# Kernel optimization log

Measured on AMD Instinct MI355X. Metric: run time of the kernel, lower is better.

## Reference

```python
import jax, jax.numpy as jnp
import numpy as np

N = 50000   # nodes
E = 1600000 # edges
G = 512     # graphs in batch
IN_DIM, EMBED, H, D = 64, 128, 4, 32
D1, D2, D3 = 128, 64, 16
NEG_SLOPE = 0.2  # DGL GATConv default


def setup_inputs() -> dict:
    key = jax.random.key(0)
    ks = jax.random.split(key, 16)
    def glorot(k, shape):
        fan = shape[0] + shape[-1]
        return jax.random.normal(k, shape, jnp.float32) * jnp.sqrt(2.0 / fan)
    return {
        "feature": jax.random.normal(ks[0], (N, IN_DIM), jnp.float32),
        "src": jax.random.randint(ks[1], (E,), 0, N, jnp.int32),
        "dst": jax.random.randint(ks[2], (E,), 0, N, jnp.int32),
        "graph_ids": jnp.sort(jax.random.randint(ks[3], (N,), 0, G, jnp.int32)),
        "W0": glorot(ks[4], (IN_DIM, EMBED)), "b0": jnp.zeros((EMBED,), jnp.float32),
        "Wfc": glorot(ks[5], (EMBED, H * D)),
        "attn_l": glorot(ks[6], (H, D)), "attn_r": glorot(ks[7], (H, D)),
        "gat_bias": jnp.zeros((H * D,), jnp.float32),
        "W1": glorot(ks[8], (H * D, D1)), "b1": jnp.zeros((D1,), jnp.float32),
        "W2": glorot(ks[9], (D1, D2)), "b2": jnp.zeros((D2,), jnp.float32),
        "W3": glorot(ks[10], (D2, D3)), "b3": jnp.zeros((D3,), jnp.float32),
    }


def reference(feature, src, dst, graph_ids, W0, b0, Wfc, attn_l, attn_r,
              gat_bias, W1, b1, W2, b2, W3, b3):
    # initial dense embed
    h = feature @ W0 + b0                                   # [N, EMBED]
    # GATConv
    feat = (h @ Wfc).reshape(N, H, D)                       # [N,H,D]
    el = jnp.einsum('nhd,hd->nh', feat, attn_l)             # [N,H]
    er = jnp.einsum('nhd,hd->nh', feat, attn_r)
    e = jax.nn.leaky_relu(el[src] + er[dst], NEG_SLOPE)     # [E,H]
    # segment softmax over incoming edges of each dst node
    m = jax.ops.segment_max(e, dst, num_segments=N)         # [N,H]
    ex = jnp.exp(e - m[dst])                                # [E,H]
    denom = jax.ops.segment_sum(ex, dst, num_segments=N)    # [N,H]
    a = ex / denom[dst]                                     # [E,H]
    msg = a[:, :, None] * feat[src]                         # [E,H,D]
    rst = jax.ops.segment_sum(msg, dst, num_segments=N)     # [N,H,D]
    rst = rst + gat_bias.reshape(1, H, D)
    hn = rst.reshape(N, H * D)
    # AvgPooling per graph
    sums = jax.ops.segment_sum(hn, graph_ids, num_segments=G)           # [G,H*D]
    cnts = jax.ops.segment_sum(jnp.ones((N,), hn.dtype), graph_ids, num_segments=G)
    hg = sums / jnp.maximum(cnts, 1.0)[:, None]
    # dense head
    out = jax.nn.elu(hg)
    out = jax.nn.elu(out @ W1 + b1)
    out = jax.nn.elu(out @ W2 + b2)
    out = out @ W3 + b3                                     # [G, D3]
    atten = a[:, :, None]                                   # [E,H,1] like DGL
    return out, atten
```

## Files before the change

kernel.cpp:

```cpp
#include <hip/hip_runtime.h>
#include <hip/hip_fp16.h>
#include <math.h>

#define N_NODES 50000
#define E_EDGES 1600000
#define G_GRAPHS 512
#define IN_DIM 64
#define EMBED 128
#define HD 128
#define NHEAD 4
#define D1 128
#define D2 64
#define D3 16
#define NEG_SLOPE 0.2f
#define NB ((N_NODES + 127) >> 7)
#define PT_TILE 4096
#define PT_BLOCKS ((E_EDGES + PT_TILE - 1) / PT_TILE)
#define FB_CAP 8192

typedef float vfloat4 __attribute__((ext_vector_type(4)));
typedef float vfloat2 __attribute__((ext_vector_type(2)));
typedef unsigned short ushort_t;

static __device__ __forceinline__ float leaky(float x) { return x > 0.f ? x : NEG_SLOPE * x; }

__global__ void __launch_bounds__(256) k0hg(const int* __restrict__ dst, int* __restrict__ ghist,
                                            const float* __restrict__ W0, const float* __restrict__ b0,
                                            const float* __restrict__ Wfc, float* __restrict__ Wc,
                                            float* __restrict__ bc) {
    __shared__ int lh[NB];
    const int t = threadIdx.x;
    if (blockIdx.x < PT_BLOCKS) {
        for (int i = t; i < NB; i += 256) lh[i] = 0;
        __syncthreads();
        const long e0 = (long)blockIdx.x * PT_TILE;
#pragma unroll
        for (int k = 0; k < PT_TILE / 256; ++k) {
            long e = e0 + t + k * 256;
            if (e < E_EDGES) atomicAdd(&lh[dst[e] >> 7], 1);
        }
        __syncthreads();
        for (int i = t; i < NB; i += 256) {
            int v = lh[i];
            if (v) atomicAdd(&ghist[i], v);
        }
    } else {
        int tid = (int)(blockIdx.x - PT_BLOCKS) * 256 + t;
        if (tid < IN_DIM * HD) {
            int i = tid >> 7, j = tid & 127;
            float acc = 0.f;
            for (int k = 0; k < EMBED; ++k) acc += W0[i * EMBED + k] * Wfc[k * HD + j];
            Wc[tid] = acc;
        } else if (tid < IN_DIM * HD + HD) {
            int j = tid - IN_DIM * HD;
            float acc = 0.f;
            for (int k = 0; k < EMBED; ++k) acc += b0[k] * Wfc[k * HD + j];
            bc[j] = acc;
        }
    }
}

__global__ void __launch_bounds__(256) k1_gemm(const float* __restrict__ A,
                                               const float* __restrict__ W,
                                               const float* __restrict__ b,
                                               const float* __restrict__ attn_l,
                                               const float* __restrict__ attn_r,
                                               unsigned char* __restrict__ feat,
                                               float* __restrict__ el,
                                               float* __restrict__ er) {
    __shared__ __align__(16) float Ws[IN_DIM * HD];
    __shared__ __align__(16) float As[64][68];
    const int t = threadIdx.x;
    const int cc = t & 31;
    const int rt = t >> 5;
    const int c0 = cc * 4;
    const int r0 = rt * 8;
    const int row0 = blockIdx.x * 64;

    {
        const float4* Wg = (const float4*)W;
        float4* Wl = (float4*)Ws;
#pragma unroll
        for (int j = 0; j < (IN_DIM * HD / 4) / 256; ++j) Wl[t + j * 256] = Wg[t + j * 256];
    }
#pragma unroll
    for (int j = 0; j < 4; ++j) {
        int i2 = t + j * 256;
        int row = i2 >> 4, kq = i2 & 15;
        int gr = row0 + row;
        float4 v = (gr < N_NODES) ? *(const float4*)(A + (size_t)gr * IN_DIM + kq * 4)
                                  : make_float4(0.f, 0.f, 0.f, 0.f);
        *(float4*)&As[row][kq * 4] = v;
    }
    __syncthreads();

    float acc[8][4];
#pragma unroll
    for (int i = 0; i < 8; ++i)
#pragma unroll
        for (int j = 0; j < 4; ++j) acc[i][j] = 0.f;

    for (int k4 = 0; k4 < IN_DIM / 4; ++k4) {
        vfloat4 w0 = *(const vfloat4*)&Ws[(k4 * 4 + 0) * HD + c0];
        vfloat4 w1 = *(const vfloat4*)&Ws[(k4 * 4 + 1) * HD + c0];
        vfloat4 w2 = *(const vfloat4*)&Ws[(k4 * 4 + 2) * HD + c0];
        vfloat4 w3 = *(const vfloat4*)&Ws[(k4 * 4 + 3) * HD + c0];
#pragma unroll
        for (int i = 0; i < 8; ++i) {
            vfloat4 a = *(const vfloat4*)&As[r0 + i][k4 * 4];
#pragma unroll
            for (int j = 0; j < 4; ++j)
                acc[i][j] += a.x * w0[j] + a.y * w1[j] + a.z * w2[j] + a.w * w3[j];
        }
    }

    {
        vfloat4 bcv = *(const vfloat4*)(b + c0);
#pragma unroll
        for (int i = 0; i < 8; ++i)
#pragma unroll
            for (int j = 0; j < 4; ++j) acc[i][j] += bcv[j];
    }

#pragma unroll
    for (int i = 0; i < 8; ++i) {
        int gr = row0 + r0 + i;
        if (gr < N_NODES) {
            unsigned int ww = __builtin_amdgcn_cvt_pk_fp8_f32(acc[i][0], acc[i][1], 0, false);
            ww = __builtin_amdgcn_cvt_pk_fp8_f32(acc[i][2], acc[i][3], ww, true);
            *(unsigned int*)(feat + (size_t)gr * HD + c0) = ww;
        }
    }

    {
        vfloat4 al = *(const vfloat4*)(attn_l + c0);
        vfloat4 ar = *(const vfloat4*)(attn_r + c0);
        float pl[8], pr[8];
#pragma unroll
        for (int i = 0; i < 8; ++i) {
            pl[i] = acc[i][0] * al[0] + acc[i][1] * al[1] + acc[i][2] * al[2] + acc[i][3] * al[3];
            pr[i] = acc[i][0] * ar[0] + acc[i][1] * ar[1] + acc[i][2] * ar[2] + acc[i][3] * ar[3];
        }
#pragma unroll
        for (int off = 1; off <= 4; off <<= 1) {
#pragma unroll
            for (int i = 0; i < 8; ++i) {
                pl[i] += __shfl_xor(pl[i], off);
                pr[i] += __shfl_xor(pr[i], off);
            }
        }
        if ((cc & 7) == 0) {
            const int h = cc >> 3;
#pragma unroll
            for (int i = 0; i < 8; ++i) {
                int gr = row0 + r0 + i;
                if (gr < N_NODES) {
                    el[gr * 4 + h] = pl[i];
                    er[gr * 4 + h] = pr[i];
                }
            }
        }
    }
}

__global__ void __launch_bounds__(64) sc_scan(const int* __restrict__ ghist,
                                              int* __restrict__ coarse_start,
                                              int* __restrict__ cursorp) {
    const int lane = threadIdx.x;
    int run = 0;
    for (int c = 0; c < (NB + 63) / 64; ++c) {
        int i = c * 64 + lane;
        int v = (i < NB) ? ghist[i] : 0;
        int incl = v;
#pragma unroll
        for (int off = 1; off < 64; off <<= 1) {
            int o = __shfl_up(incl, off, 64);
            if (lane >= off) incl += o;
        }
        if (i < NB) {
            coarse_start[i] = run + incl - v;
            cursorp[i] = run + incl - v;
        }
        run += __shfl(incl, 63, 64);
    }
    if (lane == 0) coarse_start[NB] = E_EDGES;
}

__global__ void __launch_bounds__(256) pt_partition(const int* __restrict__ src,
                                                    const int* __restrict__ dst,
                                                    int* __restrict__ cursorp,
                                                    unsigned int* __restrict__ part) {
    __shared__ int hist[4][NB];
    __shared__ int tot[NB], offs[NB], base_s[NB];
    __shared__ int lcur[4][NB];
    __shared__ unsigned int stage[PT_TILE];
    const int t = threadIdx.x, lane = t & 63, wid = t >> 6;
    const long e0 = (long)blockIdx.x * PT_TILE;
    const int cnt = (int)min((long)PT_TILE, (long)E_EDGES - e0);
    for (int i = t; i < NB; i += 256) {
        hist[0][i] = 0; hist[1][i] = 0; hist[2][i] = 0; hist[3][i] = 0;
    }
    __syncthreads();
    unsigned int v[PT_TILE / 256];
#pragma unroll
    for (int k = 0; k < PT_TILE / 256; ++k) {
        int i = t + k * 256;
        if (i < cnt) {
            int d = dst[e0 + i];
            v[k] = ((unsigned int)d << 16) | (unsigned int)src[e0 + i];
            atomicAdd(&hist[wid][d >> 7], 1);
        } else v[k] = 0xFFFFFFFFu;
    }
    __syncthreads();
    for (int i = t; i < NB; i += 256) {
        int h0 = hist[0][i], h1 = hist[1][i], h2 = hist[2][i], h3 = hist[3][i];
        hist[0][i] = 0; hist[1][i] = h0; hist[2][i] = h0 + h1; hist[3][i] = h0 + h1 + h2;
        tot[i] = h0 + h1 + h2 + h3;
    }
    __syncthreads();
    if (wid == 0) {
        int run = 0;
        for (int c = 0; c < (NB + 63) / 64; ++c) {
            int i = c * 64 + lane;
            int vv = (i < NB) ? tot[i] : 0;
            int incl = vv;
#pragma unroll
            for (int off = 1; off < 64; off <<= 1) {
                int o = __shfl_up(incl, off, 64);
                if (lane >= off) incl += o;
            }
            if (i < NB) offs[i] = run + incl - vv;
            run += __shfl(incl, 63, 64);
        }
    }
    __syncthreads();
    for (int i = t; i < NB; i += 256) {
        int tt = tot[i];
        base_s[i] = tt ? atomicAdd(&cursorp[i], tt) : 0;
        int ob = offs[i];
        lcur[0][i] = ob + hist[0][i];
        lcur[1][i] = ob + hist[1][i];
        lcur[2][i] = ob + hist[2][i];
        lcur[3][i] = ob + hist[3][i];
    }
    __syncthreads();
#pragma unroll
    for (int k = 0; k < PT_TILE / 256; ++k) {
        if (v[k] != 0xFFFFFFFFu) {
            int b = v[k] >> 23;
            int pos = atomicAdd(&lcur[wid][b], 1);
            stage[pos] = v[k];
        }
    }
    __syncthreads();
    for (int i = t; i < cnt; i += 256) {
        unsigned int p = stage[i];
        int b = p >> 23;
        part[base_s[b] + (i - offs[b])] = p & 0x7FFFFFu;
    }
}

__global__ void __launch_bounds__(256) fb_fill(const unsigned int* __restrict__ part,
                                               const int* __restrict__ coarse_start,
                                               int* __restrict__ rowstart,
                                               ushort_t* __restrict__ csr_src) {
    const int b = blockIdx.x, t = threadIdx.x, lane = t & 63, wid = t >> 6;
    const int s0 = coarse_start[b], s1 = coarse_start[b + 1];
    const int cnt = s1 - s0;
    __shared__ int degl[4][128], totl[128], offl[128], curl[4][128];
    __shared__ ushort_t lsrc[FB_CAP];
    if (t < 128) { degl[0][t] = 0; degl[1][t] = 0; degl[2][t] = 0; degl[3][t] = 0; }
    __syncthreads();
    for (int i = t; i < cnt; i += 256) {
        unsigned int p = part[s0 + i];
        atomicAdd(&degl[wid][p >> 16], 1);
    }
    __syncthreads();
    if (t < 128) {
        int d0 = degl[0][t], d1 = degl[1][t], d2 = degl[2][t], d3 = degl[3][t];
        degl[0][t] = 0; degl[1][t] = d0; degl[2][t] = d0 + d1; degl[3][t] = d0 + d1 + d2;
        totl[t] = d0 + d1 + d2 + d3;
    }
    __syncthreads();
    if (wid == 0) {
        int run = 0;
        for (int c = 0; c < 2; ++c) {
            int i = c * 64 + lane;
            int vv = totl[i];
            int incl = vv;
#pragma unroll
            for (int off = 1; off < 64; off <<= 1) {
                int o = __shfl_up(incl, off, 64);
                if (lane >= off) incl += o;
            }
            offl[i] = run + incl - vv;
            run += __shfl(incl, 63, 64);
        }
    }
    __syncthreads();
    if (t < 128) {
        int ob = offl[t];
        curl[0][t] = ob + degl[0][t];
        curl[1][t] = ob + degl[1][t];
        curl[2][t] = ob + degl[2][t];
        curl[3][t] = ob + degl[3][t];
        int node = (b << 7) + t;
        if (node < N_NODES) rowstart[node] = s0 + ob;
    }
    if (b == 0 && t == 0) rowstart[N_NODES] = E_EDGES;
    __syncthreads();
    if (cnt <= FB_CAP) {
        for (int i = t; i < cnt; i += 256) {
            unsigned int p = part[s0 + i];
            int pos = atomicAdd(&curl[wid][p >> 16], 1);
            lsrc[pos] = (ushort_t)(p & 0xFFFFu);
        }
        __syncthreads();
        for (int i = t; i < cnt; i += 256) csr_src[s0 + i] = lsrc[i];
    } else {
        for (int i = t; i < cnt; i += 256) {
            unsigned int p = part[s0 + i];
            int pos = atomicAdd(&curl[wid][p >> 16], 1);
            csr_src[s0 + pos] = (ushort_t)(p & 0xFFFFu);
        }
    }
}

__global__ void __launch_bounds__(256) k6_aggregate(
    const ushort_t* __restrict__ csr_src, const int* __restrict__ rowstart,
    const float* __restrict__ el, const float* __restrict__ er,
    const unsigned char* __restrict__ feat, const float* __restrict__ gat_bias,
    float* __restrict__ er_rd, float* __restrict__ hn) {
    __shared__ uint2 s_pk[4][64][4];
    const int wid = threadIdx.x >> 6;
    const int lane = threadIdx.x & 63;
    const int n = blockIdx.x * 4 + wid;
    if (n >= N_NODES) return;
    const int start = rowstart[n];
    const int end = rowstart[n + 1];
    const int deg = end - start;

    const int e0 = lane >> 2;
    const int h = lane & 3;
    const float erh = er[n * 4 + h];
    float sm = 0.f;
    for (int base = 0; base < deg; base += 16) {
        const int e = base + e0;
        const bool v = e < deg;
        if (v) {
            const int s = csr_src[start + e];
            const float ex = __expf(leaky(el[s * 4 + h] + erh));
            sm += ex;
            if (e < 64)
                s_pk[wid][e][h] = make_uint2((unsigned int)s << 7, __float_as_uint(ex));
        }
    }
#pragma unroll
    for (int off = 4; off <= 32; off <<= 1) sm += __shfl_xor(sm, off);
    const float rd = sm > 0.f ? 1.f / sm : 0.f;
    if (lane < 4) {
        er_rd[(size_t)n * 8 + lane] = erh;
        er_rd[(size_t)n * 8 + 4 + lane] = rd;
    }

    const int g4 = lane >> 4, gl = lane & 15;
    const int h2 = gl >> 2;
    const float rdh = __shfl(rd, h2);
    vfloat2 acc0 = {0.f, 0.f}, acc1 = {0.f, 0.f}, acc2 = {0.f, 0.f}, acc3 = {0.f, 0.f};

    if (deg <= 64) {
        const uint2* pk = &s_pk[wid][0][h2];
        const unsigned char* fg = feat + (gl << 3);
        int idx = g4;
        for (; idx + 4 < deg; idx += 8) {
            const uint2 pA = pk[idx * 4];
            const uint2 pB = pk[(idx + 4) * 4];
            const uint2 wA = *(const uint2*)(fg + pA.x);
            const uint2 wB = *(const uint2*)(fg + pB.x);
            const float exA = __uint_as_float(pA.y);
            const float exB = __uint_as_float(pB.y);
            const vfloat2 eA = {exA, exA}, eB = {exB, exB};
            acc0 += eA * __builtin_amdgcn_cvt_pk_f32_fp8(wA.x, false);
            acc1 += eA * __builtin_amdgcn_cvt_pk_f32_fp8(wA.x, true);
            acc2 += eA * __builtin_amdgcn_cvt_pk_f32_fp8(wA.y, false);
            acc3 += eA * __builtin_amdgcn_cvt_pk_f32_fp8(wA.y, true);
            acc0 += eB * __builtin_amdgcn_cvt_pk_f32_fp8(wB.x, false);
            acc1 += eB * __builtin_amdgcn_cvt_pk_f32_fp8(wB.x, true);
            acc2 += eB * __builtin_amdgcn_cvt_pk_f32_fp8(wB.y, false);
            acc3 += eB * __builtin_amdgcn_cvt_pk_f32_fp8(wB.y, true);
        }
        if (idx < deg) {
            const uint2 p = pk[idx * 4];
            const uint2 w = *(const uint2*)(fg + p.x);
            const float ex = __uint_as_float(p.y);
            const vfloat2 ev = {ex, ex};
            acc0 += ev * __builtin_amdgcn_cvt_pk_f32_fp8(w.x, false);
            acc1 += ev * __builtin_amdgcn_cvt_pk_f32_fp8(w.x, true);
            acc2 += ev * __builtin_amdgcn_cvt_pk_f32_fp8(w.y, false);
            acc3 += ev * __builtin_amdgcn_cvt_pk_f32_fp8(w.y, true);
        }
    } else {
        const float erh2 = __shfl(erh, h2);
        const unsigned char* fg = feat + (gl << 3);
        for (int e = start + g4; e < end; e += 4) {
            const unsigned int s = csr_src[e];
            const float ex = __expf(leaky(el[s * 4 + h2] + erh2));
            const vfloat2 ev = {ex, ex};
            const uint2 w = *(const uint2*)(fg + ((size_t)s << 7));
            acc0 += ev * __builtin_amdgcn_cvt_pk_f32_fp8(w.x, false);
            acc1 += ev * __builtin_amdgcn_cvt_pk_f32_fp8(w.x, true);
            acc2 += ev * __builtin_amdgcn_cvt_pk_f32_fp8(w.y, false);
            acc3 += ev * __builtin_amdgcn_cvt_pk_f32_fp8(w.y, true);
        }
    }
    {
        const vfloat2 rv = {rdh, rdh};
        acc0 *= rv; acc1 *= rv; acc2 *= rv; acc3 *= rv;
    }
#pragma unroll
    for (int off = 16; off <= 32; off <<= 1) {
        acc0.x += __shfl_xor(acc0.x, off);
        acc0.y += __shfl_xor(acc0.y, off);
        acc1.x += __shfl_xor(acc1.x, off);
        acc1.y += __shfl_xor(acc1.y, off);
        acc2.x += __shfl_xor(acc2.x, off);
        acc2.y += __shfl_xor(acc2.y, off);
        acc3.x += __shfl_xor(acc3.x, off);
        acc3.y += __shfl_xor(acc3.y, off);
    }
    if (lane < 16) {
        const float4 b0 = ((const float4*)gat_bias)[gl * 2];
        const float4 b1 = ((const float4*)gat_bias)[gl * 2 + 1];
        float4* hp = (float4*)(hn + (size_t)n * HD + gl * 8);
        hp[0] = make_float4(acc0.x + b0.x, acc0.y + b0.y, acc1.x + b0.z, acc1.y + b0.w);
        hp[1] = make_float4(acc2.x + b1.x, acc2.y + b1.y, acc3.x + b1.z, acc3.y + b1.w);
    }
}

__global__ void __launch_bounds__(256) k6b_attn(
    const int* __restrict__ src, const int* __restrict__ dst,
    const float* __restrict__ el, const float* __restrict__ er_rd,
    float* __restrict__ a_out) {
    int e = blockIdx.x * 256 + threadIdx.x;
    if (e >= E_EDGES) return;
    const int s = src[e], d = dst[e];
    const float4 el4 = *(const float4*)(el + s * 4);
    const float4 er4 = *(const float4*)(er_rd + (size_t)d * 8);
    const float4 r4 = *(const float4*)(er_rd + (size_t)d * 8 + 4);
    vfloat4 a;
    a.x = __expf(leaky(el4.x + er4.x)) * r4.x;
    a.y = __expf(leaky(el4.y + er4.y)) * r4.y;
    a.z = __expf(leaky(el4.z + er4.z)) * r4.z;
    a.w = __expf(leaky(el4.w + er4.w)) * r4.w;
    __builtin_nontemporal_store(a, (vfloat4*)a_out + e);
}

__global__ void __launch_bounds__(512) k7_pool_mlp(
    const float* __restrict__ hn, const int* __restrict__ graph_ids,
    const float* __restrict__ W1, const float* __restrict__ b1,
    const float* __restrict__ W2, const float* __restrict__ b2,
    const float* __restrict__ W3, const float* __restrict__ b3,
    float* __restrict__ out) {
    const int g = blockIdx.x, t = threadIdx.x;
    const int tt = t & 127, part = t >> 7;
    __shared__ int bounds[2];
    __shared__ double pool[4][128];
    __shared__ double x[128], y[128];
    if (t < 2) {
        const int target = g + t;
        int lo = 0, hi = N_NODES;
        while (lo < hi) {
            int mid = (lo + hi) >> 1;
            if (graph_ids[mid] < target) lo = mid + 1; else hi = mid;
        }
        bounds[t] = lo;
    }
    __syncthreads();
    const int lo = bounds[0], hi = bounds[1];
    double s = 0.0;
    for (int n = lo + part; n < hi; n += 4) s += (double)hn[(size_t)n * HD + tt];
    pool[part][tt] = s;
    __syncthreads();
    if (t < 128) {
        const double cnt = (double)(hi - lo);
        const double sum = pool[0][t] + pool[1][t] + pool[2][t] + pool[3][t];
        const double v = sum / fmax(cnt, 1.0);
        x[t] = v > 0.0 ? v : expm1(v);
    }
    __syncthreads();
    if (t < 128) {
        double acc = (double)b1[t];
        for (int k = 0; k < HD; ++k) acc += x[k] * (double)W1[k * D1 + t];
        y[t] = acc > 0.0 ? acc : expm1(acc);
    }
    __syncthreads();
    if (t < D2) {
        double a2 = (double)b2[t];
        for (int k = 0; k < D1; ++k) a2 += y[k] * (double)W2[k * D2 + t];
        x[t] = a2 > 0.0 ? a2 : expm1(a2);
    }
    __syncthreads();
    if (t < D3) {
        double a3 = (double)b3[t];
        for (int k = 0; k < D2; ++k) a3 += x[k] * (double)W3[k * D3 + t];
        out[g * D3 + t] = (float)a3;
    }
}

extern "C" void kernel_launch(void* const* d_in, const int* in_sizes, int n_in,
                              void* d_out, int out_size, void* d_ws, size_t ws_size,
                              hipStream_t stream) {
    const float* feature = (const float*)d_in[0];
    const int* src = (const int*)d_in[1];
    const int* dst = (const int*)d_in[2];
    const int* graph_ids = (const int*)d_in[3];
    const float* W0 = (const float*)d_in[4];
    const float* b0 = (const float*)d_in[5];
    const float* Wfc = (const float*)d_in[6];
    const float* attn_l = (const float*)d_in[7];
    const float* attn_r = (const float*)d_in[8];
    const float* gat_bias = (const float*)d_in[9];
    const float* W1 = (const float*)d_in[10];
    const float* b1 = (const float*)d_in[11];
    const float* W2 = (const float*)d_in[12];
    const float* b2 = (const float*)d_in[13];
    const float* W3 = (const float*)d_in[14];
    const float* b3 = (const float*)d_in[15];

    char* ws = (char*)d_ws;
    size_t off = 0;
    auto carve = [&](size_t bytes) -> void* {
        void* p = ws + off;
        off += (bytes + 255) & ~(size_t)255;
        return p;
    };
    int* ghist = (int*)carve((size_t)NB * 4);
    const size_t zero_span = off;
    int* coarse_start = (int*)carve((size_t)(NB + 1) * 4);
    int* cursorp = (int*)carve((size_t)NB * 4);
    float* Wc = (float*)carve((size_t)IN_DIM * HD * 4);
    float* bc = (float*)carve((size_t)HD * 4);
    unsigned char* feat = (unsigned char*)carve((size_t)N_NODES * HD);
    float* el = (float*)carve((size_t)N_NODES * 4 * 4);
    float* er = (float*)carve((size_t)N_NODES * 4 * 4);
    float* er_rd = (float*)carve((size_t)N_NODES * 8 * 4);
    int* rowstart = (int*)carve((size_t)(N_NODES + 1) * 4);
    unsigned int* part = (unsigned int*)carve((size_t)E_EDGES * 4);
    ushort_t* csr_src = (ushort_t*)carve((size_t)E_EDGES * 2);

    float* out = (float*)d_out;
    float* hn = out + G_GRAPHS * D3;
    float* a_out = hn;

    (void)hipMemsetAsync(d_ws, 0, zero_span, stream);
    k0hg<<<PT_BLOCKS + 33, 256, 0, stream>>>(dst, ghist, W0, b0, Wfc, Wc, bc);
    k1_gemm<<<(N_NODES + 63) / 64, 256, 0, stream>>>(feature, Wc, bc, attn_l, attn_r,
                                                     feat, el, er);
    sc_scan<<<1, 64, 0, stream>>>(ghist, coarse_start, cursorp);
    pt_partition<<<PT_BLOCKS, 256, 0, stream>>>(src, dst, cursorp, part);
    fb_fill<<<NB, 256, 0, stream>>>(part, coarse_start, rowstart, csr_src);
    k6_aggregate<<<(N_NODES + 3) / 4, 256, 0, stream>>>(csr_src, rowstart, el, er, feat,
                                                        gat_bias, er_rd, hn);
    k7_pool_mlp<<<G_GRAPHS, 512, 0, stream>>>(hn, graph_ids, W1, b1, W2, b2, W3, b3, out);
    k6b_attn<<<(E_EDGES + 255) / 256, 256, 0, stream>>>(src, dst, el, er_rd, a_out);
}
```

Measured before the change: 250.4 us.

## Fuse attention output into aggregate kernel via original-edge-index permutation

Carries each edge's original index through the partition and CSR build, so the aggregate kernel can scatter normalized attention weights straight into the output. This removes the separate per-edge attention kernel, which re-gathered el and er_rd by src and dst. It also unrolls the score computation for low-degree nodes and reshapes the feature-accumulation loop into four-wide batches. In exchange it adds 4-byte original-index streams written and read in two kernels, scattered 4-byte stores to a_out, and moves hn into the workspace.

```diff
diff --git a/kernel.cpp b/kernel.cpp
--- a/kernel.cpp
+++ b/kernel.cpp
@@ -189,11 +189,13 @@
 __global__ void __launch_bounds__(256) pt_partition(const int* __restrict__ src,
                                                     const int* __restrict__ dst,
                                                     int* __restrict__ cursorp,
-                                                    unsigned int* __restrict__ part) {
+                                                    unsigned int* __restrict__ part,
+                                                    unsigned int* __restrict__ parto) {
     __shared__ int hist[4][NB];
     __shared__ int tot[NB], offs[NB], base_s[NB];
     __shared__ int lcur[4][NB];
     __shared__ unsigned int stage[PT_TILE];
+    __shared__ unsigned int stage2[PT_TILE];
     const int t = threadIdx.x, lane = t & 63, wid = t >> 6;
     const long e0 = (long)blockIdx.x * PT_TILE;
     const int cnt = (int)min((long)PT_TILE, (long)E_EDGES - e0);
@@ -250,20 +252,25 @@
             int b = v[k] >> 23;
             int pos = atomicAdd(&lcur[wid][b], 1);
             stage[pos] = v[k];
+            stage2[pos] = (unsigned int)(e0 + t + k * 256);
         }
     }
     __syncthreads();
     for (int i = t; i < cnt; i += 256) {
         unsigned int p = stage[i];
         int b = p >> 23;
-        part[base_s[b] + (i - offs[b])] = p & 0x7FFFFFu;
+        int o = base_s[b] + (i - offs[b]);
+        part[o] = p & 0x7FFFFFu;
+        parto[o] = stage2[i];
     }
 }
 
 __global__ void __launch_bounds__(256) fb_fill(const unsigned int* __restrict__ part,
+                                               const unsigned int* __restrict__ parto,
                                                const int* __restrict__ coarse_start,
                                                int* __restrict__ rowstart,
-                                               ushort_t* __restrict__ csr_src) {
+                                               ushort_t* __restrict__ csr_src,
+                                               int* __restrict__ csr_orig) {
     const int b = blockIdx.x, t = threadIdx.x, lane = t & 63, wid = t >> 6;
     const int s0 = coarse_start[b], s1 = coarse_start[b + 1];
     const int cnt = s1 - s0;
@@ -312,25 +319,30 @@
     if (cnt <= FB_CAP) {
         for (int i = t; i < cnt; i += 256) {
             unsigned int p = part[s0 + i];
+            int orig = (int)parto[s0 + i];
             int pos = atomicAdd(&curl[wid][p >> 16], 1);
             lsrc[pos] = (ushort_t)(p & 0xFFFFu);
+            csr_orig[s0 + pos] = orig;
         }
         __syncthreads();
         for (int i = t; i < cnt; i += 256) csr_src[s0 + i] = lsrc[i];
     } else {
         for (int i = t; i < cnt; i += 256) {
             unsigned int p = part[s0 + i];
+            int orig = (int)parto[s0 + i];
             int pos = atomicAdd(&curl[wid][p >> 16], 1);
             csr_src[s0 + pos] = (ushort_t)(p & 0xFFFFu);
+            csr_orig[s0 + pos] = orig;
         }
     }
 }
 
 __global__ void __launch_bounds__(256) k6_aggregate(
-    const ushort_t* __restrict__ csr_src, const int* __restrict__ rowstart,
+    const ushort_t* __restrict__ csr_src, const int* __restrict__ csr_orig,
+    const int* __restrict__ rowstart,
     const float* __restrict__ el, const float* __restrict__ er,
     const unsigned char* __restrict__ feat, const float* __restrict__ gat_bias,
-    float* __restrict__ er_rd, float* __restrict__ hn) {
+    float* __restrict__ hn, float* __restrict__ a_out) {
     __shared__ uint2 s_pk[4][64][4];
     const int wid = threadIdx.x >> 6;
     const int lane = threadIdx.x & 63;
@@ -344,23 +356,66 @@
     const int h = lane & 3;
     const float erh = er[n * 4 + h];
     float sm = 0.f;
-    for (int base = 0; base < deg; base += 16) {
-        const int e = base + e0;
-        const bool v = e < deg;
-        if (v) {
-            const int s = csr_src[start + e];
-            const float ex = __expf(leaky(el[s * 4 + h] + erh));
-            sm += ex;
-            if (e < 64)
-                s_pk[wid][e][h] = make_uint2((unsigned int)s << 7, __float_as_uint(ex));
+    bool vA = false, vB = false, vC = false, vD = false;
+    float xA = 0.f, xB = 0.f, xC = 0.f, xD = 0.f;
+    int oA = 0, oB = 0, oC = 0, oD = 0;
+    if (deg <= 64) {
+        vA = e0 < deg; vB = e0 + 16 < deg; vC = e0 + 32 < deg; vD = e0 + 48 < deg;
+        const int iA = start + (vA ? e0 : 0);
+        const int iB = start + (vB ? e0 + 16 : 0);
+        const int iC = start + (vC ? e0 + 32 : 0);
+        const int iD = start + (vD ? e0 + 48 : 0);
+        const int sA = csr_src[iA], sB = csr_src[iB], sC = csr_src[iC], sD = csr_src[iD];
+        oA = csr_orig[iA]; oB = csr_orig[iB]; oC = csr_orig[iC]; oD = csr_orig[iD];
+        const float lA = el[sA * 4 + h];
+        const float lB = el[sB * 4 + h];
+        const float lC = el[sC * 4 + h];
+        const float lD = el[sD * 4 + h];
+        xA = vA ? __expf(leaky(lA + erh)) : 0.f;
+        xB = vB ? __expf(leaky(lB + erh)) : 0.f;
+        xC = vC ? __expf(leaky(lC + erh)) : 0.f;
+        xD = vD ? __expf(leaky(lD + erh)) : 0.f;
+        sm = xA + xB + xC + xD;
+        if (vA) s_pk[wid][e0][h]      = make_uint2((unsigned int)sA << 7, __float_as_uint(xA));
+        if (vB) s_pk[wid][e0 + 16][h] = make_uint2((unsigned int)sB << 7, __float_as_uint(xB));
+        if (vC) s_pk[wid][e0 + 32][h] = make_uint2((unsigned int)sC << 7, __float_as_uint(xC));
+        if (vD) s_pk[wid][e0 + 48][h] = make_uint2((unsigned int)sD << 7, __float_as_uint(xD));
+    } else {
+        for (int base = 0; base < deg; base += 16) {
+            const int e = base + e0;
+            if (e < deg) {
+                const int s = csr_src[start + e];
+                const float ex = __expf(leaky(el[s * 4 + h] + erh));
+                sm += ex;
+                if (e < 64)
+                    s_pk[wid][e][h] = make_uint2((unsigned int)s << 7, __float_as_uint(ex));
+            }
         }
     }
 #pragma unroll
     for (int off = 4; off <= 32; off <<= 1) sm += __shfl_xor(sm, off);
     const float rd = sm > 0.f ? 1.f / sm : 0.f;
-    if (lane < 4) {
-        er_rd[(size_t)n * 8 + lane] = erh;
-        er_rd[(size_t)n * 8 + 4 + lane] = rd;
+
+    if (deg <= 64) {
+        if (vA) a_out[(size_t)oA * 4 + h] = xA * rd;
+        if (vB) a_out[(size_t)oB * 4 + h] = xB * rd;
+        if (vC) a_out[(size_t)oC * 4 + h] = xC * rd;
+        if (vD) a_out[(size_t)oD * 4 + h] = xD * rd;
+    } else {
+        const float er0 = __shfl(erh, 0), er1 = __shfl(erh, 1);
+        const float er2 = __shfl(erh, 2), er3 = __shfl(erh, 3);
+        const float rd0 = __shfl(rd, 0), rd1 = __shfl(rd, 1);
+        const float rd2 = __shfl(rd, 2), rd3 = __shfl(rd, 3);
+        for (int e = start + lane; e < end; e += 64) {
+            const int s = csr_src[e], o = csr_orig[e];
+            const float4 elv = *(const float4*)(el + s * 4);
+            vfloat4 a;
+            a.x = __expf(leaky(elv.x + er0)) * rd0;
+            a.y = __expf(leaky(elv.y + er1)) * rd1;
+            a.z = __expf(leaky(elv.z + er2)) * rd2;
+            a.w = __expf(leaky(elv.w + er3)) * rd3;
+            *(vfloat4*)(a_out + (size_t)o * 4) = a;
+        }
     }
 
     const int g4 = lane >> 4, gl = lane & 15;
@@ -371,33 +426,50 @@
     if (deg <= 64) {
         const uint2* pk = &s_pk[wid][0][h2];
         const unsigned char* fg = feat + (gl << 3);
-        int idx = g4;
-        for (; idx + 4 < deg; idx += 8) {
-            const uint2 pA = pk[idx * 4];
-            const uint2 pB = pk[(idx + 4) * 4];
-            const uint2 wA = *(const uint2*)(fg + pA.x);
-            const uint2 wB = *(const uint2*)(fg + pB.x);
-            const float exA = __uint_as_float(pA.y);
-            const float exB = __uint_as_float(pB.y);
-            const vfloat2 eA = {exA, exA}, eB = {exB, exB};
-            acc0 += eA * __builtin_amdgcn_cvt_pk_f32_fp8(wA.x, false);
-            acc1 += eA * __builtin_amdgcn_cvt_pk_f32_fp8(wA.x, true);
-            acc2 += eA * __builtin_amdgcn_cvt_pk_f32_fp8(wA.y, false);
-            acc3 += eA * __builtin_amdgcn_cvt_pk_f32_fp8(wA.y, true);
-            acc0 += eB * __builtin_amdgcn_cvt_pk_f32_fp8(wB.x, false);
-            acc1 += eB * __builtin_amdgcn_cvt_pk_f32_fp8(wB.x, true);
-            acc2 += eB * __builtin_amdgcn_cvt_pk_f32_fp8(wB.y, false);
-            acc3 += eB * __builtin_amdgcn_cvt_pk_f32_fp8(wB.y, true);
-        }
-        if (idx < deg) {
-            const uint2 p = pk[idx * 4];
-            const uint2 w = *(const uint2*)(fg + p.x);
-            const float ex = __uint_as_float(p.y);
-            const vfloat2 ev = {ex, ex};
-            acc0 += ev * __builtin_amdgcn_cvt_pk_f32_fp8(w.x, false);
-            acc1 += ev * __builtin_amdgcn_cvt_pk_f32_fp8(w.x, true);
-            acc2 += ev * __builtin_amdgcn_cvt_pk_f32_fp8(w.y, false);
-            acc3 += ev * __builtin_amdgcn_cvt_pk_f32_fp8(w.y, true);
+        for (int base = g4; base < deg; base += 16) {
+            const int E1 = base + 4 < deg ? base + 4 : base;
+            const int E2 = base + 8 < deg ? base + 8 : base;
+            const int E3 = base + 12 < deg ? base + 12 : base;
+            const uint2 p0 = pk[base * 4];
+            const uint2 p1 = pk[E1 * 4];
+            const uint2 p2 = pk[E2 * 4];
+            const uint2 p3 = pk[E3 * 4];
+            const uint2 w0 = *(const uint2*)(fg + p0.x);
+            const uint2 w1 = *(const uint2*)(fg + p1.x);
+            const uint2 w2 = *(const uint2*)(fg + p2.x);
+            const uint2 w3 = *(const uint2*)(fg + p3.x);
+            const float y0 = __uint_as_float(p0.y);
+            const float y1 = base + 4 < deg ? __uint_as_float(p1.y) : 0.f;
+            const float y2 = base + 8 < deg ? __uint_as_float(p2.y) : 0.f;
+            const float y3 = base + 12 < deg ? __uint_as_float(p3.y) : 0.f;
+            {
+                const vfloat2 e = {y0, y0};
+                acc0 += e * __builtin_amdgcn_cvt_pk_f32_fp8(w0.x, false);
+                acc1 += e * __builtin_amdgcn_cvt_pk_f32_fp8(w0.x, true);
+                acc2 += e * __builtin_amdgcn_cvt_pk_f32_fp8(w0.y, false);
+                acc3 += e * __builtin_amdgcn_cvt_pk_f32_fp8(w0.y, true);
+            }
+            {
+                const vfloat2 e = {y1, y1};
+                acc0 += e * __builtin_amdgcn_cvt_pk_f32_fp8(w1.x, false);
+                acc1 += e * __builtin_amdgcn_cvt_pk_f32_fp8(w1.x, true);
+                acc2 += e * __builtin_amdgcn_cvt_pk_f32_fp8(w1.y, false);
+                acc3 += e * __builtin_amdgcn_cvt_pk_f32_fp8(w1.y, true);
+            }
+            {
+                const vfloat2 e = {y2, y2};
+                acc0 += e * __builtin_amdgcn_cvt_pk_f32_fp8(w2.x, false);
+                acc1 += e * __builtin_amdgcn_cvt_pk_f32_fp8(w2.x, true);
+                acc2 += e * __builtin_amdgcn_cvt_pk_f32_fp8(w2.y, false);
+                acc3 += e * __builtin_amdgcn_cvt_pk_f32_fp8(w2.y, true);
+            }
+            {
+                const vfloat2 e = {y3, y3};
+                acc0 += e * __builtin_amdgcn_cvt_pk_f32_fp8(w3.x, false);
+                acc1 += e * __builtin_amdgcn_cvt_pk_f32_fp8(w3.x, true);
+                acc2 += e * __builtin_amdgcn_cvt_pk_f32_fp8(w3.y, false);
+                acc3 += e * __builtin_amdgcn_cvt_pk_f32_fp8(w3.y, true);
+            }
         }
     } else {
         const float erh2 = __shfl(erh, h2);
@@ -435,24 +507,6 @@
         hp[0] = make_float4(acc0.x + b0.x, acc0.y + b0.y, acc1.x + b0.z, acc1.y + b0.w);
         hp[1] = make_float4(acc2.x + b1.x, acc2.y + b1.y, acc3.x + b1.z, acc3.y + b1.w);
     }
-}
-
-__global__ void __launch_bounds__(256) k6b_attn(
-    const int* __restrict__ src, const int* __restrict__ dst,
-    const float* __restrict__ el, const float* __restrict__ er_rd,
-    float* __restrict__ a_out) {
-    int e = blockIdx.x * 256 + threadIdx.x;
-    if (e >= E_EDGES) return;
-    const int s = src[e], d = dst[e];
-    const float4 el4 = *(const float4*)(el + s * 4);
-    const float4 er4 = *(const float4*)(er_rd + (size_t)d * 8);
-    const float4 r4 = *(const float4*)(er_rd + (size_t)d * 8 + 4);
-    vfloat4 a;
-    a.x = __expf(leaky(el4.x + er4.x)) * r4.x;
-    a.y = __expf(leaky(el4.y + er4.y)) * r4.y;
-    a.z = __expf(leaky(el4.z + er4.z)) * r4.z;
-    a.w = __expf(leaky(el4.w + er4.w)) * r4.w;
-    __builtin_nontemporal_store(a, (vfloat4*)a_out + e);
 }
 
 __global__ void __launch_bounds__(512) k7_pool_mlp(
@@ -543,24 +597,24 @@
     unsigned char* feat = (unsigned char*)carve((size_t)N_NODES * HD);
     float* el = (float*)carve((size_t)N_NODES * 4 * 4);
     float* er = (float*)carve((size_t)N_NODES * 4 * 4);
-    float* er_rd = (float*)carve((size_t)N_NODES * 8 * 4);
     int* rowstart = (int*)carve((size_t)(N_NODES + 1) * 4);
     unsigned int* part = (unsigned int*)carve((size_t)E_EDGES * 4);
+    unsigned int* parto = (unsigned int*)carve((size_t)E_EDGES * 4);
     ushort_t* csr_src = (ushort_t*)carve((size_t)E_EDGES * 2);
+    int* csr_orig = (int*)carve((size_t)E_EDGES * 4);
+    float* hn = (float*)carve((size_t)N_NODES * HD * 4);
 
     float* out = (float*)d_out;
-    float* hn = out + G_GRAPHS * D3;
-    float* a_out = hn;
+    float* a_out = out + G_GRAPHS * D3;
 
     (void)hipMemsetAsync(d_ws, 0, zero_span, stream);
     k0hg<<<PT_BLOCKS + 33, 256, 0, stream>>>(dst, ghist, W0, b0, Wfc, Wc, bc);
     k1_gemm<<<(N_NODES + 63) / 64, 256, 0, stream>>>(feature, Wc, bc, attn_l, attn_r,
                                                      feat, el, er);
     sc_scan<<<1, 64, 0, stream>>>(ghist, coarse_start, cursorp);
-    pt_partition<<<PT_BLOCKS, 256, 0, stream>>>(src, dst, cursorp, part);
-    fb_fill<<<NB, 256, 0, stream>>>(part, coarse_start, rowstart, csr_src);
-    k6_aggregate<<<(N_NODES + 3) / 4, 256, 0, stream>>>(csr_src, rowstart, el, er, feat,
-                                                        gat_bias, er_rd, hn);
+    pt_partition<<<PT_BLOCKS, 256, 0, stream>>>(src, dst, cursorp, part, parto);
+    fb_fill<<<NB, 256, 0, stream>>>(part, parto, coarse_start, rowstart, csr_src, csr_orig);
+    k6_aggregate<<<(N_NODES + 3) / 4, 256, 0, stream>>>(csr_src, csr_orig, rowstart, el, er,
+                                                        feat, gat_bias, hn, a_out);
     k7_pool_mlp<<<G_GRAPHS, 512, 0, stream>>>(hn, graph_ids, W1, b1, W2, b2, W3, b3, out);
-    k6b_attn<<<(E_EDGES + 255) / 256, 256, 0, stream>>>(src, dst, el, er_rd, a_out);
-}
+}
```

Result: no change. 248.0 us (-1.0%).

## Split GAT aggregation into two head-halves per node, unroll edge loads

Applied to the files above, without the earlier changes.

The aggregation kernel now launches twice as many blocks, and each half handles two of the four heads (64 feature bytes) per destination node. The softmax-denominator pass for low-degree nodes is unrolled into four independent gathers, and the weighted-sum loop issues four loads per iteration to expose more memory parallelism. fb_fill now processes two coarse buckets per block, and the partition tile is doubled. The cost is that each half recomputes the edge exponentials and denominators, and CSR indices are read twice.

```diff
diff --git a/kernel.cpp b/kernel.cpp
--- a/kernel.cpp
+++ b/kernel.cpp
@@ -14,9 +14,10 @@
 #define D3 16
 #define NEG_SLOPE 0.2f
 #define NB ((N_NODES + 127) >> 7)
-#define PT_TILE 4096
+#define PT_TILE 8192
 #define PT_BLOCKS ((E_EDGES + PT_TILE - 1) / PT_TILE)
 #define FB_CAP 8192
+#define K6_NBLK ((N_NODES + 3) / 4)
 
 typedef float vfloat4 __attribute__((ext_vector_type(4)));
 typedef float vfloat2 __attribute__((ext_vector_type(2)));
@@ -264,65 +265,70 @@
                                                const int* __restrict__ coarse_start,
                                                int* __restrict__ rowstart,
                                                ushort_t* __restrict__ csr_src) {
-    const int b = blockIdx.x, t = threadIdx.x, lane = t & 63, wid = t >> 6;
-    const int s0 = coarse_start[b], s1 = coarse_start[b + 1];
-    const int cnt = s1 - s0;
+    const int t = threadIdx.x, lane = t & 63, wid = t >> 6;
     __shared__ int degl[4][128], totl[128], offl[128], curl[4][128];
     __shared__ ushort_t lsrc[FB_CAP];
-    if (t < 128) { degl[0][t] = 0; degl[1][t] = 0; degl[2][t] = 0; degl[3][t] = 0; }
-    __syncthreads();
-    for (int i = t; i < cnt; i += 256) {
-        unsigned int p = part[s0 + i];
-        atomicAdd(&degl[wid][p >> 16], 1);
-    }
-    __syncthreads();
-    if (t < 128) {
-        int d0 = degl[0][t], d1 = degl[1][t], d2 = degl[2][t], d3 = degl[3][t];
-        degl[0][t] = 0; degl[1][t] = d0; degl[2][t] = d0 + d1; degl[3][t] = d0 + d1 + d2;
-        totl[t] = d0 + d1 + d2 + d3;
-    }
-    __syncthreads();
-    if (wid == 0) {
-        int run = 0;
-        for (int c = 0; c < 2; ++c) {
-            int i = c * 64 + lane;
-            int vv = totl[i];
-            int incl = vv;
-#pragma unroll
-            for (int off = 1; off < 64; off <<= 1) {
-                int o = __shfl_up(incl, off, 64);
-                if (lane >= off) incl += o;
-            }
-            offl[i] = run + incl - vv;
-            run += __shfl(incl, 63, 64);
-        }
-    }
-    __syncthreads();
-    if (t < 128) {
-        int ob = offl[t];
-        curl[0][t] = ob + degl[0][t];
-        curl[1][t] = ob + degl[1][t];
-        curl[2][t] = ob + degl[2][t];
-        curl[3][t] = ob + degl[3][t];
-        int node = (b << 7) + t;
-        if (node < N_NODES) rowstart[node] = s0 + ob;
-    }
-    if (b == 0 && t == 0) rowstart[N_NODES] = E_EDGES;
-    __syncthreads();
-    if (cnt <= FB_CAP) {
+    if (blockIdx.x == 0 && t == 0) rowstart[N_NODES] = E_EDGES;
+    for (int sub = 0; sub < 2; ++sub) {
+        const int b = (int)blockIdx.x * 2 + sub;
+        if (b >= NB) break;
+        const int s0 = coarse_start[b], s1 = coarse_start[b + 1];
+        const int cnt = s1 - s0;
+        if (t < 128) { degl[0][t] = 0; degl[1][t] = 0; degl[2][t] = 0; degl[3][t] = 0; }
+        __syncthreads();
         for (int i = t; i < cnt; i += 256) {
             unsigned int p = part[s0 + i];
-            int pos = atomicAdd(&curl[wid][p >> 16], 1);
-            lsrc[pos] = (ushort_t)(p & 0xFFFFu);
-        }
-        __syncthreads();
-        for (int i = t; i < cnt; i += 256) csr_src[s0 + i] = lsrc[i];
-    } else {
-        for (int i = t; i < cnt; i += 256) {
-            unsigned int p = part[s0 + i];
-            int pos = atomicAdd(&curl[wid][p >> 16], 1);
-            csr_src[s0 + pos] = (ushort_t)(p & 0xFFFFu);
-        }
+            atomicAdd(&degl[wid][p >> 16], 1);
+        }
+        __syncthreads();
+        if (t < 128) {
+            int d0 = degl[0][t], d1 = degl[1][t], d2 = degl[2][t], d3 = degl[3][t];
+            degl[0][t] = 0; degl[1][t] = d0; degl[2][t] = d0 + d1; degl[3][t] = d0 + d1 + d2;
+            totl[t] = d0 + d1 + d2 + d3;
+        }
+        __syncthreads();
+        if (wid == 0) {
+            int run = 0;
+            for (int c = 0; c < 2; ++c) {
+                int i = c * 64 + lane;
+                int vv = totl[i];
+                int incl = vv;
+#pragma unroll
+                for (int off = 1; off < 64; off <<= 1) {
+                    int o = __shfl_up(incl, off, 64);
+                    if (lane >= off) incl += o;
+                }
+                offl[i] = run + incl - vv;
+                run += __shfl(incl, 63, 64);
+            }
+        }
+        __syncthreads();
+        if (t < 128) {
+            int ob = offl[t];
+            curl[0][t] = ob + degl[0][t];
+            curl[1][t] = ob + degl[1][t];
+            curl[2][t] = ob + degl[2][t];
+            curl[3][t] = ob + degl[3][t];
+            int node = (b << 7) + t;
+            if (node < N_NODES) rowstart[node] = s0 + ob;
+        }
+        __syncthreads();
+        if (cnt <= FB_CAP) {
+            for (int i = t; i < cnt; i += 256) {
+                unsigned int p = part[s0 + i];
+                int pos = atomicAdd(&curl[wid][p >> 16], 1);
+                lsrc[pos] = (ushort_t)(p & 0xFFFFu);
+            }
+            __syncthreads();
+            for (int i = t; i < cnt; i += 256) csr_src[s0 + i] = lsrc[i];
+        } else {
+            for (int i = t; i < cnt; i += 256) {
+                unsigned int p = part[s0 + i];
+                int pos = atomicAdd(&curl[wid][p >> 16], 1);
+                csr_src[s0 + pos] = (ushort_t)(p & 0xFFFFu);
+            }
+        }
+        __syncthreads();
     }
 }
 
@@ -334,7 +340,8 @@
     __shared__ uint2 s_pk[4][64][4];
     const int wid = threadIdx.x >> 6;
     const int lane = threadIdx.x & 63;
-    const int n = blockIdx.x * 4 + wid;
+    const int half = (int)(blockIdx.x >= K6_NBLK);
+    const int n = ((int)blockIdx.x - half * K6_NBLK) * 4 + wid;
     if (n >= N_NODES) return;
     const int start = rowstart[n];
     const int end = rowstart[n + 1];
@@ -344,78 +351,106 @@
     const int h = lane & 3;
     const float erh = er[n * 4 + h];
     float sm = 0.f;
-    for (int base = 0; base < deg; base += 16) {
-        const int e = base + e0;
-        const bool v = e < deg;
-        if (v) {
-            const int s = csr_src[start + e];
-            const float ex = __expf(leaky(el[s * 4 + h] + erh));
-            sm += ex;
-            if (e < 64)
-                s_pk[wid][e][h] = make_uint2((unsigned int)s << 7, __float_as_uint(ex));
+    if (deg <= 64) {
+        const bool vA = e0 < deg, vB = e0 + 16 < deg, vC = e0 + 32 < deg, vD = e0 + 48 < deg;
+        const int iA = start + (vA ? e0 : 0);
+        const int iB = start + (vB ? e0 + 16 : 0);
+        const int iC = start + (vC ? e0 + 32 : 0);
+        const int iD = start + (vD ? e0 + 48 : 0);
+        const int sA = csr_src[iA], sB = csr_src[iB], sC = csr_src[iC], sD = csr_src[iD];
+        const float lA = el[sA * 4 + h];
+        const float lB = el[sB * 4 + h];
+        const float lC = el[sC * 4 + h];
+        const float lD = el[sD * 4 + h];
+        const float xA = vA ? __expf(leaky(lA + erh)) : 0.f;
+        const float xB = vB ? __expf(leaky(lB + erh)) : 0.f;
+        const float xC = vC ? __expf(leaky(lC + erh)) : 0.f;
+        const float xD = vD ? __expf(leaky(lD + erh)) : 0.f;
+        sm = xA + xB + xC + xD;
+        if (vA) s_pk[wid][e0][h]      = make_uint2((unsigned int)sA << 7, __float_as_uint(xA));
+        if (vB) s_pk[wid][e0 + 16][h] = make_uint2((unsigned int)sB << 7, __float_as_uint(xB));
+        if (vC) s_pk[wid][e0 + 32][h] = make_uint2((unsigned int)sC << 7, __float_as_uint(xC));
+        if (vD) s_pk[wid][e0 + 48][h] = make_uint2((unsigned int)sD << 7, __float_as_uint(xD));
+    } else {
+        for (int base = 0; base < deg; base += 16) {
+            const int e = base + e0;
+            if (e < deg) {
+                const int s = csr_src[start + e];
+                const float ex = __expf(leaky(el[s * 4 + h] + erh));
+                sm += ex;
+                if (e < 64)
+                    s_pk[wid][e][h] = make_uint2((unsigned int)s << 7, __float_as_uint(ex));
+            }
         }
     }
 #pragma unroll
     for (int off = 4; off <= 32; off <<= 1) sm += __shfl_xor(sm, off);
     const float rd = sm > 0.f ? 1.f / sm : 0.f;
-    if (lane < 4) {
+    if (half == 0 && lane < 4) {
         er_rd[(size_t)n * 8 + lane] = erh;
         er_rd[(size_t)n * 8 + 4 + lane] = rd;
     }
 
     const int g4 = lane >> 4, gl = lane & 15;
-    const int h2 = gl >> 2;
+    const int h2 = (half << 1) | (gl >> 3);
     const float rdh = __shfl(rd, h2);
-    vfloat2 acc0 = {0.f, 0.f}, acc1 = {0.f, 0.f}, acc2 = {0.f, 0.f}, acc3 = {0.f, 0.f};
+    vfloat2 acc0 = {0.f, 0.f}, acc1 = {0.f, 0.f};
 
     if (deg <= 64) {
         const uint2* pk = &s_pk[wid][0][h2];
-        const unsigned char* fg = feat + (gl << 3);
-        int idx = g4;
-        for (; idx + 4 < deg; idx += 8) {
-            const uint2 pA = pk[idx * 4];
-            const uint2 pB = pk[(idx + 4) * 4];
-            const uint2 wA = *(const uint2*)(fg + pA.x);
-            const uint2 wB = *(const uint2*)(fg + pB.x);
-            const float exA = __uint_as_float(pA.y);
-            const float exB = __uint_as_float(pB.y);
-            const vfloat2 eA = {exA, exA}, eB = {exB, exB};
-            acc0 += eA * __builtin_amdgcn_cvt_pk_f32_fp8(wA.x, false);
-            acc1 += eA * __builtin_amdgcn_cvt_pk_f32_fp8(wA.x, true);
-            acc2 += eA * __builtin_amdgcn_cvt_pk_f32_fp8(wA.y, false);
-            acc3 += eA * __builtin_amdgcn_cvt_pk_f32_fp8(wA.y, true);
-            acc0 += eB * __builtin_amdgcn_cvt_pk_f32_fp8(wB.x, false);
-            acc1 += eB * __builtin_amdgcn_cvt_pk_f32_fp8(wB.x, true);
-            acc2 += eB * __builtin_amdgcn_cvt_pk_f32_fp8(wB.y, false);
-            acc3 += eB * __builtin_amdgcn_cvt_pk_f32_fp8(wB.y, true);
-        }
-        if (idx < deg) {
-            const uint2 p = pk[idx * 4];
-            const uint2 w = *(const uint2*)(fg + p.x);
-            const float ex = __uint_as_float(p.y);
-            const vfloat2 ev = {ex, ex};
-            acc0 += ev * __builtin_amdgcn_cvt_pk_f32_fp8(w.x, false);
-            acc1 += ev * __builtin_amdgcn_cvt_pk_f32_fp8(w.x, true);
-            acc2 += ev * __builtin_amdgcn_cvt_pk_f32_fp8(w.y, false);
-            acc3 += ev * __builtin_amdgcn_cvt_pk_f32_fp8(w.y, true);
+        const unsigned char* fg = feat + half * 64 + (gl << 2);
+        for (int base = g4; base < deg; base += 16) {
+            const int E1 = base + 4 < deg ? base + 4 : base;
+            const int E2 = base + 8 < deg ? base + 8 : base;
+            const int E3 = base + 12 < deg ? base + 12 : base;
+            const uint2 p0 = pk[base * 4];
+            const uint2 p1 = pk[E1 * 4];
+            const uint2 p2 = pk[E2 * 4];
+            const uint2 p3 = pk[E3 * 4];
+            const unsigned int w0 = *(const unsigned int*)(fg + p0.x);
+            const unsigned int w1 = *(const unsigned int*)(fg + p1.x);
+            const unsigned int w2 = *(const unsigned int*)(fg + p2.x);
+            const unsigned int w3 = *(const unsigned int*)(fg + p3.x);
+            const float y0 = __uint_as_float(p0.y);
+            const float y1 = base + 4 < deg ? __uint_as_float(p1.y) : 0.f;
+            const float y2 = base + 8 < deg ? __uint_as_float(p2.y) : 0.f;
+            const float y3 = base + 12 < deg ? __uint_as_float(p3.y) : 0.f;
+            {
+                const vfloat2 e = {y0, y0};
+                acc0 += e * __builtin_amdgcn_cvt_pk_f32_fp8(w0, false);
+                acc1 += e * __builtin_amdgcn_cvt_pk_f32_fp8(w0, true);
+            }
+            {
+                const vfloat2 e = {y1, y1};
+                acc0 += e * __builtin_amdgcn_cvt_pk_f32_fp8(w1, false);
+                acc1 += e * __builtin_amdgcn_cvt_pk_f32_fp8(w1, true);
+            }
+            {
+                const vfloat2 e = {y2, y2};
+                acc0 += e * __builtin_amdgcn_cvt_pk_f32_fp8(w2, false);
+                acc1 += e * __builtin_amdgcn_cvt_pk_f32_fp8(w2, true);
+            }
+            {
+                const vfloat2 e = {y3, y3};
+                acc0 += e * __builtin_amdgcn_cvt_pk_f32_fp8(w3, false);
+                acc1 += e * __builtin_amdgcn_cvt_pk_f32_fp8(w3, true);
+            }
         }
     } else {
         const float erh2 = __shfl(erh, h2);
-        const unsigned char* fg = feat + (gl << 3);
+        const unsigned char* fg = feat + half * 64 + (gl << 2);
         for (int e = start + g4; e < end; e += 4) {
             const unsigned int s = csr_src[e];
             const float ex = __expf(leaky(el[s * 4 + h2] + erh2));
             const vfloat2 ev = {ex, ex};
-            const uint2 w = *(const uint2*)(fg + ((size_t)s << 7));
-            acc0 += ev * __builtin_amdgcn_cvt_pk_f32_fp8(w.x, false);
-            acc1 += ev * __builtin_amdgcn_cvt_pk_f32_fp8(w.x, true);
-            acc2 += ev * __builtin_amdgcn_cvt_pk_f32_fp8(w.y, false);
-            acc3 += ev * __builtin_amdgcn_cvt_pk_f32_fp8(w.y, true);
+            const unsigned int w = *(const unsigned int*)(fg + ((size_t)s << 7));
+            acc0 += ev * __builtin_amdgcn_cvt_pk_f32_fp8(w, false);
+            acc1 += ev * __builtin_amdgcn_cvt_pk_f32_fp8(w, true);
         }
     }
     {
         const vfloat2 rv = {rdh, rdh};
-        acc0 *= rv; acc1 *= rv; acc2 *= rv; acc3 *= rv;
+        acc0 *= rv; acc1 *= rv;
     }
 #pragma unroll
     for (int off = 16; off <= 32; off <<= 1) {
@@ -423,17 +458,11 @@
         acc0.y += __shfl_xor(acc0.y, off);
         acc1.x += __shfl_xor(acc1.x, off);
         acc1.y += __shfl_xor(acc1.y, off);
-        acc2.x += __shfl_xor(acc2.x, off);
-        acc2.y += __shfl_xor(acc2.y, off);
-        acc3.x += __shfl_xor(acc3.x, off);
-        acc3.y += __shfl_xor(acc3.y, off);
     }
     if (lane < 16) {
-        const float4 b0 = ((const float4*)gat_bias)[gl * 2];
-        const float4 b1 = ((const float4*)gat_bias)[gl * 2 + 1];
-        float4* hp = (float4*)(hn + (size_t)n * HD + gl * 8);
-        hp[0] = make_float4(acc0.x + b0.x, acc0.y + b0.y, acc1.x + b0.z, acc1.y + b0.w);
-        hp[1] = make_float4(acc2.x + b1.x, acc2.y + b1.y, acc3.x + b1.z, acc3.y + b1.w);
+        const float4 bq = ((const float4*)gat_bias)[half * 16 + gl];
+        *(float4*)(hn + (size_t)n * HD + half * 64 + gl * 4) =
+            make_float4(acc0.x + bq.x, acc0.y + bq.y, acc1.x + bq.z, acc1.y + bq.w);
     }
 }
 
@@ -558,9 +587,9 @@
                                                      feat, el, er);
     sc_scan<<<1, 64, 0, stream>>>(ghist, coarse_start, cursorp);
     pt_partition<<<PT_BLOCKS, 256, 0, stream>>>(src, dst, cursorp, part);
-    fb_fill<<<NB, 256, 0, stream>>>(part, coarse_start, rowstart, csr_src);
-    k6_aggregate<<<(N_NODES + 3) / 4, 256, 0, stream>>>(csr_src, rowstart, el, er, feat,
-                                                        gat_bias, er_rd, hn);
+    fb_fill<<<(NB + 1) / 2, 256, 0, stream>>>(part, coarse_start, rowstart, csr_src);
+    k6_aggregate<<<2 * K6_NBLK, 256, 0, stream>>>(csr_src, rowstart, el, er, feat,
+                                                  gat_bias, er_rd, hn);
     k7_pool_mlp<<<G_GRAPHS, 512, 0, stream>>>(hn, graph_ids, W1, b1, W2, b2, W3, b3, out);
     k6b_attn<<<(E_EDGES + 255) / 256, 256, 0, stream>>>(src, dst, el, er_rd, a_out);
 }
```

After: 269.9 us. 7.8% more time.
